# Kernel optimization log

Measured on AMD Instinct MI355X. Metric: run time of the kernel, lower is better.

Reference implementation:

```python
import jax, jax.numpy as jnp
import numpy as np

B, P, EPG = 1000, 100, 1200  # graphs, nodes/graph, edges/graph
IN, HID, OUT, K = 16, 64, 5, 3


def setup_inputs() -> dict:
    key = jax.random.key(0)
    ks = jax.random.split(key, 12)
    offs = jnp.repeat(jnp.arange(B, dtype=jnp.int32) * P, EPG)
    src = jax.random.randint(ks[0], (B * EPG,), 0, P, dtype=jnp.int32) + offs
    dst = jax.random.randint(ks[1], (B * EPG,), 0, P, dtype=jnp.int32) + offs
    graph_ids = jnp.repeat(jnp.arange(B, dtype=jnp.int32), P)
    feat = jax.random.normal(ks[2], (B * P, IN), dtype=jnp.float32)

    def lin(k1, fan_in, fan_out):
        s = 1.0 / np.sqrt(fan_in)
        return jax.random.uniform(k1, (fan_in, fan_out), jnp.float32, -s, s)

    return {
        'feat': feat, 'src': src, 'dst': dst, 'graph_ids': graph_ids,
        'n_graphs': B,
        'W1': lin(ks[3], K * IN, HID), 'b1': jnp.zeros((HID,), jnp.float32),
        'W2': lin(ks[4], K * HID, HID), 'b2': jnp.zeros((HID,), jnp.float32),
        'W3': lin(ks[5], K * HID, HID), 'b3': jnp.zeros((HID,), jnp.float32),
        'Wfc': lin(ks[6], HID, OUT), 'bfc': jnp.zeros((OUT,), jnp.float32),
    }


def _cheb_conv(x, src, dst, d_invsqrt, W, b, k):
    # DGL ChebConv with lambda_max=2 -> re_norm=1, scaled Laplacian = -D^-1/2 A D^-1/2
    n = x.shape[0]

    def Ax(h):
        msg = (h * d_invsqrt)[src]                      # gather from source nodes
        agg = jax.ops.segment_sum(msg, dst, num_segments=n)
        return agg * d_invsqrt

    Xs = [x]
    if k > 1:
        Xs.append(-Ax(Xs[0]))                           # X1 = L_hat X0
        for _ in range(2, k):
            Xs.append(-2.0 * Ax(Xs[-1]) - Xs[-2])       # X_i = 2 L_hat X_{i-1} - X_{i-2}
    Xt = jnp.concatenate(Xs, axis=1)                    # [n, k*f]
    return Xt @ W + b


def reference(feat, src, dst, graph_ids, n_graphs, W1, b1, W2, b2, W3, b3, Wfc, bfc):
    n = feat.shape[0]
    deg = jax.ops.segment_sum(jnp.ones((src.shape[0],), feat.dtype), dst, num_segments=n)
    d_invsqrt = jnp.where(deg < 1.0, 1.0, deg) ** -0.5
    d_invsqrt = d_invsqrt[:, None]

    h = jax.nn.relu(_cheb_conv(feat, src, dst, d_invsqrt, W1, b1, K))
    h = jax.nn.relu(_cheb_conv(h, src, dst, d_invsqrt, W2, b2, K))
    h = jax.nn.relu(_cheb_conv(h, src, dst, d_invsqrt, W3, b3, K))

    # dgl.mean_nodes: per-graph mean pooling
    counts = jax.ops.segment_sum(jnp.ones((n,), h.dtype), graph_ids, num_segments=n_graphs)
    hg = jax.ops.segment_sum(h, graph_ids, num_segments=n_graphs) / counts[:, None]
    return hg @ Wfc + bfc
```

## Files before the change

kernel.cpp:

```cpp
#include <hip/hip_runtime.h>

#define NGRAPH 1000
#define P      100
#define EPG    1200
#define INF    16
#define HID    64
#define NOUT   5

#define ASTR   88
#define T2OFF  72
#define SLOTA  64
#define SLOTB  80
#define NPAD   112


typedef short short8 __attribute__((ext_vector_type(8)));
typedef float f32x4  __attribute__((ext_vector_type(4)));

__device__ __forceinline__ void bsplit(float x, short& h, short& l) {
    unsigned u = __float_as_uint(x);
    h = (short)(u >> 16);
    float hf = __uint_as_float(u & 0xffff0000u);
    l = (short)(__float_as_uint(x - hf) >> 16);
}

__global__ __launch_bounds__(256) void wprep(
    const float* __restrict__ W1, const float* __restrict__ W2,
    const float* __restrict__ W3, short* __restrict__ wt)
{
    const int i0 = blockIdx.x * blockDim.x + threadIdx.x;
    const int stride = gridDim.x * blockDim.x;
    for (int e = i0; e < HID * 56; e += stride) {
        int c = e / 56, r = e % 56;
        float v = (r < 48) ? W1[r * HID + c] : 0.f;
        short h, l; bsplit(v, h, l);
        wt[e]        = h;
        wt[3584 + e] = l;
    }
    for (int e = i0; e < HID * 200; e += stride) {
        int c = e / 200, r = e % 200;
        float v2 = (r < 192) ? W2[r * HID + c] : 0.f;
        float v3 = (r < 192) ? W3[r * HID + c] : 0.f;
        short h, l;
        bsplit(v2, h, l); wt[7168 + e]  = h; wt[19968 + e] = l;
        bsplit(v3, h, l); wt[32768 + e] = h; wt[45568 + e] = l;
    }
}

__device__ __forceinline__ void prop_x1(
    float* __restrict__ A, int soff, int dslot,
    const unsigned char* __restrict__ csr_src,
    const int* __restrict__ csr_off,
    const float* __restrict__ dinv, int tid)
{
    const int q4 = (tid & 1) * 4;
    const int n  = tid >> 1;
    if (n < P) {
        const int kb = csr_off[n], ke = csr_off[n + 1];
        float ax = 0.f, ay = 0.f, az = 0.f, aw = 0.f;
        for (int k = kb; k < ke; k++) {
            int s = csr_src[k];
            const float4 x = *(const float4*)&A[s * ASTR + soff + q4];
            ax += x.x; ay += x.y; az += x.z; aw += x.w;
        }
        float dn = dinv[n];
        float m = -dn * dn;
        float4 o; o.x = m * ax; o.y = m * ay; o.z = m * az; o.w = m * aw;
        *(float4*)&A[n * ASTR + dslot + q4] = o;
    }
}

__device__ __forceinline__ void prop_dual(
    float* __restrict__ A, int t1c, int t1n, int ycur, int ynext, bool pre,
    const unsigned char* __restrict__ csr_src,
    const int* __restrict__ csr_off,
    const float* __restrict__ dinv, int tid)
{
    const int q4 = (tid & 1) * 4;
    const int n  = tid >> 1;
    if (n < P) {
        const int kb = csr_off[n], ke = csr_off[n + 1];
        float4 a2 = make_float4(0.f, 0.f, 0.f, 0.f);
        float4 a1 = make_float4(0.f, 0.f, 0.f, 0.f);
        if (pre) {
            for (int k = kb; k < ke; k++) {
                int s = csr_src[k];
                const float* rp = &A[s * ASTR + q4];
                const float4 x2 = *(const float4*)&rp[t1c];
                const float4 x1 = *(const float4*)&rp[ynext];
                a2.x += x2.x; a2.y += x2.y; a2.z += x2.z; a2.w += x2.w;
                a1.x += x1.x; a1.y += x1.y; a1.z += x1.z; a1.w += x1.w;
            }
        } else {
            for (int k = kb; k < ke; k++) {
                int s = csr_src[k];
                const float4 x2 = *(const float4*)&A[s * ASTR + t1c + q4];
                a2.x += x2.x; a2.y += x2.y; a2.z += x2.z; a2.w += x2.w;
            }
        }
        float dn = dinv[n];
        float d2 = dn * dn;
        const float4 y0 = *(const float4*)&A[n * ASTR + ycur + q4];
        float4 o2;
        float m2 = -2.f * d2;
        o2.x = m2 * a2.x - y0.x; o2.y = m2 * a2.y - y0.y;
        o2.z = m2 * a2.z - y0.z; o2.w = m2 * a2.w - y0.w;
        *(float4*)&A[n * ASTR + T2OFF + q4] = o2;
        if (pre) {
            float m1 = -d2;
            float4 o1;
            o1.x = m1 * a1.x; o1.y = m1 * a1.y;
            o1.z = m1 * a1.z; o1.w = m1 * a1.w;
            *(float4*)&A[n * ASTR + t1n + q4] = o1;
        }
    }
}

template <int F, int FINAL>
__device__ __forceinline__ void cheb_layer(
    float* __restrict__ A,
    const unsigned char* __restrict__ csr_src,
    const int* __restrict__ csr_off,
    const float* __restrict__ dinv,
    const short* __restrict__ whi, const short* __restrict__ wlo,
    const float* __restrict__ bias, int tid)
{
    const int RK   = 3 * F + 8;
    const int lane = tid & 63;
    const int wv   = tid >> 6;
    const int n16  = lane & 15;
    const int q    = lane >> 4;
    const int ncol = (wv << 4) + n16;

    f32x4 acc[7];
#pragma unroll
    for (int t = 0; t < 7; t++) { acc[t][0]=0.f; acc[t][1]=0.f; acc[t][2]=0.f; acc[t][3]=0.f; }

    prop_x1(A, 0, SLOTA, csr_src, csr_off, dinv, tid);
    __syncthreads();

    int t1c = SLOTA, t1n = SLOTB;
    for (int cb = 0; cb < F; cb += 8) {
        const bool pre = (cb + 8 < F);
        prop_dual(A, t1c, t1n, cb, cb + 8, pre, csr_src, csr_off, dinv, tid);
        __syncthreads();

        const int wr = (q == 0) ? cb : (q == 1) ? (F + cb)
                     : (q == 2) ? (2 * F + cb) : (3 * F);
        const short8 bhi = *(const short8*)&whi[ncol * RK + wr];
        const short8 blo = *(const short8*)&wlo[ncol * RK + wr];

        const int aoff = (q == 0) ? cb : (q == 1) ? t1c
                       : (q == 2) ? T2OFF : cb;
#pragma unroll
        for (int t = 0; t < 7; t++) {
            const float* xp = &A[(t * 16 + n16) * ASTR + aoff];
            const float4 v0 = *(const float4*)xp;
            const float4 v1 = *(const float4*)(xp + 4);
            short8 ahi, alo; short h, l;
            bsplit(v0.x, h, l); ahi[0] = h; alo[0] = l;
            bsplit(v0.y, h, l); ahi[1] = h; alo[1] = l;
            bsplit(v0.z, h, l); ahi[2] = h; alo[2] = l;
            bsplit(v0.w, h, l); ahi[3] = h; alo[3] = l;
            bsplit(v1.x, h, l); ahi[4] = h; alo[4] = l;
            bsplit(v1.y, h, l); ahi[5] = h; alo[5] = l;
            bsplit(v1.z, h, l); ahi[6] = h; alo[6] = l;
            bsplit(v1.w, h, l); ahi[7] = h; alo[7] = l;
            acc[t] = __builtin_amdgcn_mfma_f32_16x16x32_bf16(ahi, bhi, acc[t], 0, 0, 0);
            acc[t] = __builtin_amdgcn_mfma_f32_16x16x32_bf16(ahi, blo, acc[t], 0, 0, 0);
            acc[t] = __builtin_amdgcn_mfma_f32_16x16x32_bf16(alo, bhi, acc[t], 0, 0, 0);
        }
        __syncthreads();
        int tt = t1c; t1c = t1n; t1n = tt;
    }

    const float bcol = bias[ncol];
    const int rbase = q * 4;
#pragma unroll
    for (int t = 0; t < 7; t++) {
#pragma unroll
        for (int r = 0; r < 4; r++) {
            int row = t * 16 + rbase + r;
            if (row < P) {
                float dn = dinv[row];
                float v = acc[t][r];
                float o;
                if (FINAL) o = fmaxf(v * (1.0f / dn) + bcol, 0.f);
                else       o = fmaxf(v + bcol * dn, 0.f);
                A[row * ASTR + ncol] = o;
            }
        }
    }
    __syncthreads();
}

__global__ __launch_bounds__(256, 4) void gnn_kernel(
    const float* __restrict__ feat,
    const int* __restrict__ src, const int* __restrict__ dst,
    const float* __restrict__ b1, const float* __restrict__ b2,
    const float* __restrict__ b3,
    const float* __restrict__ Wfc, const float* __restrict__ bfc,
    const short* __restrict__ wt,
    float* __restrict__ out)
{
    __shared__ __align__(16) float A[NPAD * ASTR];
    __shared__ unsigned char csr_src[EPG];

    const int g = blockIdx.x;
    const int tid = threadIdx.x;
    const int base = g * P;
    const int* srcg = src + g * EPG;
    const int* dstg = dst + g * EPG;

    int*   deg     = (int*)&A[P * ASTR];
    int*   cur     = (int*)&A[P * ASTR + 100];
    int*   csr_off = (int*)&A[P * ASTR + 200];
    float* dinv    = &A[P * ASTR + 304];
    float* psum    = &A[P * ASTR + 404];

    for (int i = tid; i < P; i += 256) deg[i] = 0;
    __syncthreads();
    for (int e = tid; e < EPG; e += 256) {
        int d = dstg[e] - base;
        atomicAdd(&deg[d], 1);
    }
    __syncthreads();

    for (int i = tid; i < P; i += 256) {
        int dg = deg[i] > 1 ? deg[i] : 1;
        dinv[i] = rsqrtf((float)dg);
    }
    if (tid == 0) {
        int run = 0;
        csr_off[0] = 0;
        for (int i = 0; i < P; i++) { run += deg[i]; csr_off[i + 1] = run; }
    }
    __syncthreads();

    for (int i = tid; i < P * INF / 4; i += 256) {
        int n = i >> 2, fq = (i & 3) * 4;
        float4 v = *(const float4*)&feat[(size_t)base * INF + i * 4];
        float dn = dinv[n];
        v.x *= dn; v.y *= dn; v.z *= dn; v.w *= dn;
        *(float4*)&A[n * ASTR + fq] = v;
    }
    for (int i = tid; i < P; i += 256) cur[i] = csr_off[i];
    __syncthreads();
    for (int e = tid; e < EPG; e += 256) {
        int s = srcg[e] - base;
        int d = dstg[e] - base;
        int pos = atomicAdd(&cur[d], 1);
        csr_src[pos] = (unsigned char)s;
    }
    __syncthreads();

    cheb_layer<INF, 0>(A, csr_src, csr_off, dinv, wt,         wt + 3584,  b1, tid);
    cheb_layer<HID, 0>(A, csr_src, csr_off, dinv, wt + 7168,  wt + 19968, b2, tid);
    cheb_layer<HID, 1>(A, csr_src, csr_off, dinv, wt + 32768, wt + 45568, b3, tid);

    {
        const int lane = tid & 63, w = tid >> 6;
        float s = 0.f;
        for (int n = w; n < P; n += 4) s += A[n * ASTR + lane];
        psum[w * 64 + lane] = s;
    }
    __syncthreads();
    if (tid < HID) {
        float hg = (psum[tid] + psum[64 + tid] + psum[128 + tid] + psum[192 + tid]) * (1.0f / P);
        psum[256 + tid] = hg;
    }
    __syncthreads();
    if (tid < NOUT) {
        float o = bfc[tid];
        for (int c = 0; c < HID; c++) o += psum[256 + c] * Wfc[c * NOUT + tid];
        out[g * NOUT + tid] = o;
    }
}

extern "C" void kernel_launch(void* const* d_in, const int* in_sizes, int n_in,
                              void* d_out, int out_size, void* d_ws, size_t ws_size,
                              hipStream_t stream)
{
    const float* feat = (const float*)d_in[0];
    const int*   src  = (const int*)d_in[1];
    const int*   dst  = (const int*)d_in[2];
    const float* W1  = (const float*)d_in[5];
    const float* b1  = (const float*)d_in[6];
    const float* W2  = (const float*)d_in[7];
    const float* b2  = (const float*)d_in[8];
    const float* W3  = (const float*)d_in[9];
    const float* b3  = (const float*)d_in[10];
    const float* Wfc = (const float*)d_in[11];
    const float* bfc = (const float*)d_in[12];
    float* out = (float*)d_out;
    short* wt = (short*)d_ws;

    wprep<<<64, 256, 0, stream>>>(W1, W2, W3, wt);
    gnn_kernel<<<NGRAPH, 256, 0, stream>>>(feat, src, dst,
                                           b1, b2, b3, Wfc, bfc, wt, out);
}
```

Baseline: 186.8 us.

## Replace CSR sparse propagation with dense per-graph adjacency MFMA products

A new kernel builds each graph's dense 100x128 adjacency count matrix as bf16 in global workspace. The main kernel then computes the Laplacian propagation as MFMA matrix products against split-bf16 features instead of per-node CSR gather loops. Propagation now runs in 16-column chunks with an enlarged shared row stride that also holds degree and dinv, dropping the CSR build and the serial prefix scan. The cost is about 25 MB of extra adjacency traffic through global memory, an extra launch, and more MFMA work on a mostly zero matrix.

```diff
diff --git a/kernel.cpp b/kernel.cpp
--- a/kernel.cpp
+++ b/kernel.cpp
@@ -7,12 +7,25 @@
 #define HID    64
 #define NOUT   5
 
-#define ASTR   88
-#define T2OFF  72
-#define SLOTA  64
-#define SLOTB  80
-#define NPAD   112
-
+
+#define ASTR   100
+#define DINVC  64
+#define DEGC   65
+#define T1OFF  68
+#define T2OFF  84
+
+#define AINT_K   128
+#define AINT_SZ  (P * AINT_K)
+
+#define RK1    64
+#define RK2    208
+#define L1HI   0
+#define L1LO   4096
+#define L2HI   8192
+#define L2LO   21504
+#define L3HI   34816
+#define L3LO   48128
+#define WT_SHORTS 61440
 
 typedef short short8 __attribute__((ext_vector_type(8)));
 typedef float f32x4  __attribute__((ext_vector_type(4)));
@@ -30,160 +43,179 @@
 {
     const int i0 = blockIdx.x * blockDim.x + threadIdx.x;
     const int stride = gridDim.x * blockDim.x;
-    for (int e = i0; e < HID * 56; e += stride) {
-        int c = e / 56, r = e % 56;
-        float v = (r < 48) ? W1[r * HID + c] : 0.f;
+    for (int e = i0; e < HID * RK1; e += stride) {
+        int c = e / RK1, r = e % RK1;
+        float v = (r < 3 * INF) ? W1[r * HID + c] : 0.f;
         short h, l; bsplit(v, h, l);
-        wt[e]        = h;
-        wt[3584 + e] = l;
-    }
-    for (int e = i0; e < HID * 200; e += stride) {
-        int c = e / 200, r = e % 200;
-        float v2 = (r < 192) ? W2[r * HID + c] : 0.f;
-        float v3 = (r < 192) ? W3[r * HID + c] : 0.f;
+        wt[L1HI + e] = h;
+        wt[L1LO + e] = l;
+    }
+    for (int e = i0; e < HID * RK2; e += stride) {
+        int c = e / RK2, r = e % RK2;
+        float v2 = (r < 3 * HID) ? W2[r * HID + c] : 0.f;
+        float v3 = (r < 3 * HID) ? W3[r * HID + c] : 0.f;
         short h, l;
-        bsplit(v2, h, l); wt[7168 + e]  = h; wt[19968 + e] = l;
-        bsplit(v3, h, l); wt[32768 + e] = h; wt[45568 + e] = l;
-    }
-}
-
-__device__ __forceinline__ void prop_x1(
-    float* __restrict__ A, int soff, int dslot,
-    const unsigned char* __restrict__ csr_src,
-    const int* __restrict__ csr_off,
-    const float* __restrict__ dinv, int tid)
-{
-    const int q4 = (tid & 1) * 4;
-    const int n  = tid >> 1;
-    if (n < P) {
-        const int kb = csr_off[n], ke = csr_off[n + 1];
-        float ax = 0.f, ay = 0.f, az = 0.f, aw = 0.f;
-        for (int k = kb; k < ke; k++) {
-            int s = csr_src[k];
-            const float4 x = *(const float4*)&A[s * ASTR + soff + q4];
-            ax += x.x; ay += x.y; az += x.z; aw += x.w;
-        }
-        float dn = dinv[n];
-        float m = -dn * dn;
-        float4 o; o.x = m * ax; o.y = m * ay; o.z = m * az; o.w = m * aw;
-        *(float4*)&A[n * ASTR + dslot + q4] = o;
-    }
-}
-
-__device__ __forceinline__ void prop_dual(
-    float* __restrict__ A, int t1c, int t1n, int ycur, int ynext, bool pre,
-    const unsigned char* __restrict__ csr_src,
-    const int* __restrict__ csr_off,
-    const float* __restrict__ dinv, int tid)
-{
-    const int q4 = (tid & 1) * 4;
-    const int n  = tid >> 1;
-    if (n < P) {
-        const int kb = csr_off[n], ke = csr_off[n + 1];
-        float4 a2 = make_float4(0.f, 0.f, 0.f, 0.f);
-        float4 a1 = make_float4(0.f, 0.f, 0.f, 0.f);
-        if (pre) {
-            for (int k = kb; k < ke; k++) {
-                int s = csr_src[k];
-                const float* rp = &A[s * ASTR + q4];
-                const float4 x2 = *(const float4*)&rp[t1c];
-                const float4 x1 = *(const float4*)&rp[ynext];
-                a2.x += x2.x; a2.y += x2.y; a2.z += x2.z; a2.w += x2.w;
-                a1.x += x1.x; a1.y += x1.y; a1.z += x1.z; a1.w += x1.w;
+        bsplit(v2, h, l); wt[L2HI + e] = h; wt[L2LO + e] = l;
+        bsplit(v3, h, l); wt[L3HI + e] = h; wt[L3LO + e] = l;
+    }
+}
+
+__global__ __launch_bounds__(256) void abuild(
+    const int* __restrict__ src, const int* __restrict__ dst,
+    short* __restrict__ aint)
+{
+    __shared__ unsigned int cnt[AINT_SZ / 2];
+    const int g = blockIdx.x, tid = threadIdx.x, base = g * P;
+    for (int i = tid; i < AINT_SZ / 2; i += 256) cnt[i] = 0u;
+    __syncthreads();
+    const int* srcg = src + g * EPG;
+    const int* dstg = dst + g * EPG;
+    for (int e = tid; e < EPG; e += 256) {
+        int s = srcg[e] - base;
+        int d = dstg[e] - base;
+        int idx = d * AINT_K + s;
+        atomicAdd(&cnt[idx >> 1], 1u << ((idx & 1) * 16));
+    }
+    __syncthreads();
+    unsigned int* outw = (unsigned int*)(aint + (size_t)g * AINT_SZ);
+    for (int i = tid; i < AINT_SZ / 2; i += 256) {
+        unsigned int u = cnt[i];
+        unsigned int b0 = __float_as_uint((float)(u & 0xffffu)) >> 16;
+        unsigned int b1 = __float_as_uint((float)(u >> 16)) >> 16;
+        outw[i] = b0 | (b1 << 16);
+    }
+}
+
+template <int SECOND>
+__device__ __forceinline__ void dense_prop(
+    float* __restrict__ A, const short* __restrict__ aintg,
+    int arow0, int arow1, bool has2,
+    int srcoff, int dstoff, int ycol,
+    int rb0, int rb1, f32x4 dv0, f32x4 dv1, int lane)
+{
+    const int n16 = lane & 15;
+    const int q   = lane >> 4;
+    const int kq  = q * 8;
+    f32x4 p0, p1;
+    p0[0]=0.f; p0[1]=0.f; p0[2]=0.f; p0[3]=0.f;
+    p1[0]=0.f; p1[1]=0.f; p1[2]=0.f; p1[3]=0.f;
+#pragma unroll
+    for (int k = 0; k < 4; k++) {
+        const short8 a0 = *(const short8*)&aintg[arow0 * AINT_K + k * 32 + kq];
+        const short8 a1 = *(const short8*)&aintg[arow1 * AINT_K + k * 32 + kq];
+        short8 bhi, blo; short h, l;
+#pragma unroll
+        for (int j = 0; j < 8; j++) {
+            int row = k * 32 + kq + j;
+            if (k == 3) row = (row < P) ? row : 0;
+            float x = A[row * ASTR + srcoff + n16];
+            bsplit(x, h, l); bhi[j] = h; blo[j] = l;
+        }
+        p0 = __builtin_amdgcn_mfma_f32_16x16x32_bf16(a0, bhi, p0, 0, 0, 0);
+        p0 = __builtin_amdgcn_mfma_f32_16x16x32_bf16(a0, blo, p0, 0, 0, 0);
+        if (has2) {
+            p1 = __builtin_amdgcn_mfma_f32_16x16x32_bf16(a1, bhi, p1, 0, 0, 0);
+            p1 = __builtin_amdgcn_mfma_f32_16x16x32_bf16(a1, blo, p1, 0, 0, 0);
+        }
+    }
+#pragma unroll
+    for (int r = 0; r < 4; r++) {
+        const int row = rb0 + q * 4 + r;
+        const float d2 = dv0[r] * dv0[r];
+        float o;
+        if (SECOND) o = -2.f * d2 * p0[r] - A[row * ASTR + ycol];
+        else        o = -d2 * p0[r];
+        A[row * ASTR + dstoff + n16] = o;
+    }
+    if (has2) {
+#pragma unroll
+        for (int r = 0; r < 4; r++) {
+            const int row = rb1 + q * 4 + r;
+            if (rb1 != 84 || row >= 96) {
+                const float d2 = dv1[r] * dv1[r];
+                float o;
+                if (SECOND) o = -2.f * d2 * p1[r] - A[row * ASTR + ycol];
+                else        o = -d2 * p1[r];
+                A[row * ASTR + dstoff + n16] = o;
             }
-        } else {
-            for (int k = kb; k < ke; k++) {
-                int s = csr_src[k];
-                const float4 x2 = *(const float4*)&A[s * ASTR + t1c + q4];
-                a2.x += x2.x; a2.y += x2.y; a2.z += x2.z; a2.w += x2.w;
-            }
-        }
-        float dn = dinv[n];
-        float d2 = dn * dn;
-        const float4 y0 = *(const float4*)&A[n * ASTR + ycur + q4];
-        float4 o2;
-        float m2 = -2.f * d2;
-        o2.x = m2 * a2.x - y0.x; o2.y = m2 * a2.y - y0.y;
-        o2.z = m2 * a2.z - y0.z; o2.w = m2 * a2.w - y0.w;
-        *(float4*)&A[n * ASTR + T2OFF + q4] = o2;
-        if (pre) {
-            float m1 = -d2;
-            float4 o1;
-            o1.x = m1 * a1.x; o1.y = m1 * a1.y;
-            o1.z = m1 * a1.z; o1.w = m1 * a1.w;
-            *(float4*)&A[n * ASTR + t1n + q4] = o1;
         }
     }
 }
 
 template <int F, int FINAL>
 __device__ __forceinline__ void cheb_layer(
-    float* __restrict__ A,
-    const unsigned char* __restrict__ csr_src,
-    const int* __restrict__ csr_off,
-    const float* __restrict__ dinv,
+    float* __restrict__ A, const short* __restrict__ aintg,
     const short* __restrict__ whi, const short* __restrict__ wlo,
-    const float* __restrict__ bias, int tid)
-{
-    const int RK   = 3 * F + 8;
+    const float* __restrict__ bias,
+    int tid, int rb0, int rb1, bool has2, f32x4 dv0, f32x4 dv1)
+{
+    const int RK   = 3 * F + 16;
     const int lane = tid & 63;
     const int wv   = tid >> 6;
     const int n16  = lane & 15;
     const int q    = lane >> 4;
     const int ncol = (wv << 4) + n16;
 
+    const int arow0 = rb0 + n16;
+    const int arow1 = (has2 ? rb1 : rb0) + n16;
+
     f32x4 acc[7];
 #pragma unroll
     for (int t = 0; t < 7; t++) { acc[t][0]=0.f; acc[t][1]=0.f; acc[t][2]=0.f; acc[t][3]=0.f; }
 
-    prop_x1(A, 0, SLOTA, csr_src, csr_off, dinv, tid);
-    __syncthreads();
-
-    int t1c = SLOTA, t1n = SLOTB;
-    for (int cb = 0; cb < F; cb += 8) {
-        const bool pre = (cb + 8 < F);
-        prop_dual(A, t1c, t1n, cb, cb + 8, pre, csr_src, csr_off, dinv, tid);
+    for (int cb = 0; cb < F; cb += 16) {
+        dense_prop<0>(A, aintg, arow0, arow1, has2, cb, T1OFF, cb + n16,
+                      rb0, rb1, dv0, dv1, lane);
         __syncthreads();
-
-        const int wr = (q == 0) ? cb : (q == 1) ? (F + cb)
-                     : (q == 2) ? (2 * F + cb) : (3 * F);
-        const short8 bhi = *(const short8*)&whi[ncol * RK + wr];
-        const short8 blo = *(const short8*)&wlo[ncol * RK + wr];
-
-        const int aoff = (q == 0) ? cb : (q == 1) ? t1c
-                       : (q == 2) ? T2OFF : cb;
-#pragma unroll
-        for (int t = 0; t < 7; t++) {
-            const float* xp = &A[(t * 16 + n16) * ASTR + aoff];
-            const float4 v0 = *(const float4*)xp;
-            const float4 v1 = *(const float4*)(xp + 4);
-            short8 ahi, alo; short h, l;
-            bsplit(v0.x, h, l); ahi[0] = h; alo[0] = l;
-            bsplit(v0.y, h, l); ahi[1] = h; alo[1] = l;
-            bsplit(v0.z, h, l); ahi[2] = h; alo[2] = l;
-            bsplit(v0.w, h, l); ahi[3] = h; alo[3] = l;
-            bsplit(v1.x, h, l); ahi[4] = h; alo[4] = l;
-            bsplit(v1.y, h, l); ahi[5] = h; alo[5] = l;
-            bsplit(v1.z, h, l); ahi[6] = h; alo[6] = l;
-            bsplit(v1.w, h, l); ahi[7] = h; alo[7] = l;
-            acc[t] = __builtin_amdgcn_mfma_f32_16x16x32_bf16(ahi, bhi, acc[t], 0, 0, 0);
-            acc[t] = __builtin_amdgcn_mfma_f32_16x16x32_bf16(ahi, blo, acc[t], 0, 0, 0);
-            acc[t] = __builtin_amdgcn_mfma_f32_16x16x32_bf16(alo, bhi, acc[t], 0, 0, 0);
-        }
+        dense_prop<1>(A, aintg, arow0, arow1, has2, T1OFF, T2OFF, cb + n16,
+                      rb0, rb1, dv0, dv1, lane);
         __syncthreads();
-        int tt = t1c; t1c = t1n; t1n = tt;
+
+#pragma unroll
+        for (int ks = 0; ks < 2; ks++) {
+            int wr, aoff;
+            if (ks == 0) {
+                wr   = (q == 0) ? cb : (q == 1) ? cb + 8 : (q == 2) ? F + cb : F + cb + 8;
+                aoff = (q == 0) ? cb : (q == 1) ? cb + 8 : (q == 2) ? T1OFF  : T1OFF + 8;
+            } else {
+                wr   = (q == 0) ? 2*F + cb : (q == 1) ? 2*F + cb + 8 : (q == 2) ? 3*F : 3*F + 8;
+                aoff = (q == 0) ? T2OFF    : (q == 1) ? T2OFF + 8    : (q == 2) ? T1OFF : T1OFF + 8;
+            }
+            const short8 bhi = *(const short8*)&whi[ncol * RK + wr];
+            const short8 blo = *(const short8*)&wlo[ncol * RK + wr];
+#pragma unroll
+            for (int t = 0; t < 7; t++) {
+                const int row = ((t < 6) ? t * 16 : 84) + n16;
+                const float* xp = &A[row * ASTR + aoff];
+                const float4 v0 = *(const float4*)xp;
+                const float4 v1 = *(const float4*)(xp + 4);
+                short8 ahi, alo; short h, l;
+                bsplit(v0.x, h, l); ahi[0] = h; alo[0] = l;
+                bsplit(v0.y, h, l); ahi[1] = h; alo[1] = l;
+                bsplit(v0.z, h, l); ahi[2] = h; alo[2] = l;
+                bsplit(v0.w, h, l); ahi[3] = h; alo[3] = l;
+                bsplit(v1.x, h, l); ahi[4] = h; alo[4] = l;
+                bsplit(v1.y, h, l); ahi[5] = h; alo[5] = l;
+                bsplit(v1.z, h, l); ahi[6] = h; alo[6] = l;
+                bsplit(v1.w, h, l); ahi[7] = h; alo[7] = l;
+                acc[t] = __builtin_amdgcn_mfma_f32_16x16x32_bf16(ahi, bhi, acc[t], 0, 0, 0);
+                acc[t] = __builtin_amdgcn_mfma_f32_16x16x32_bf16(ahi, blo, acc[t], 0, 0, 0);
+                acc[t] = __builtin_amdgcn_mfma_f32_16x16x32_bf16(alo, bhi, acc[t], 0, 0, 0);
+            }
+        }
+        __syncthreads();
     }
 
     const float bcol = bias[ncol];
-    const int rbase = q * 4;
 #pragma unroll
     for (int t = 0; t < 7; t++) {
+        const int rbase = ((t < 6) ? t * 16 : 84) + q * 4;
 #pragma unroll
         for (int r = 0; r < 4; r++) {
-            int row = t * 16 + rbase + r;
-            if (row < P) {
-                float dn = dinv[row];
-                float v = acc[t][r];
+            const int row = rbase + r;
+            if (t < 6 || row >= 96) {
+                const float dn = A[row * ASTR + DINVC];
+                const float v = acc[t][r];
                 float o;
                 if (FINAL) o = fmaxf(v * (1.0f / dn) + bcol, 0.f);
                 else       o = fmaxf(v + bcol * dn, 0.f);
@@ -200,79 +232,70 @@
     const float* __restrict__ b1, const float* __restrict__ b2,
     const float* __restrict__ b3,
     const float* __restrict__ Wfc, const float* __restrict__ bfc,
-    const short* __restrict__ wt,
+    const short* __restrict__ wt, const short* __restrict__ aint,
     float* __restrict__ out)
 {
-    __shared__ __align__(16) float A[NPAD * ASTR];
-    __shared__ unsigned char csr_src[EPG];
-
+    __shared__ __align__(16) float A[P * ASTR];
     const int g = blockIdx.x;
     const int tid = threadIdx.x;
     const int base = g * P;
-    const int* srcg = src + g * EPG;
     const int* dstg = dst + g * EPG;
 
-    int*   deg     = (int*)&A[P * ASTR];
-    int*   cur     = (int*)&A[P * ASTR + 100];
-    int*   csr_off = (int*)&A[P * ASTR + 200];
-    float* dinv    = &A[P * ASTR + 304];
-    float* psum    = &A[P * ASTR + 404];
-
-    for (int i = tid; i < P; i += 256) deg[i] = 0;
+    for (int i = tid; i < P; i += 256) *(int*)&A[i * ASTR + DEGC] = 0;
     __syncthreads();
     for (int e = tid; e < EPG; e += 256) {
         int d = dstg[e] - base;
-        atomicAdd(&deg[d], 1);
-    }
-    __syncthreads();
-
+        atomicAdd((int*)&A[d * ASTR + DEGC], 1);
+    }
+    __syncthreads();
     for (int i = tid; i < P; i += 256) {
-        int dg = deg[i] > 1 ? deg[i] : 1;
-        dinv[i] = rsqrtf((float)dg);
-    }
-    if (tid == 0) {
-        int run = 0;
-        csr_off[0] = 0;
-        for (int i = 0; i < P; i++) { run += deg[i]; csr_off[i + 1] = run; }
+        int dg = *(int*)&A[i * ASTR + DEGC];
+        A[i * ASTR + DINVC] = rsqrtf((float)(dg > 1 ? dg : 1));
     }
     __syncthreads();
 
     for (int i = tid; i < P * INF / 4; i += 256) {
         int n = i >> 2, fq = (i & 3) * 4;
         float4 v = *(const float4*)&feat[(size_t)base * INF + i * 4];
-        float dn = dinv[n];
+        float dn = A[n * ASTR + DINVC];
         v.x *= dn; v.y *= dn; v.z *= dn; v.w *= dn;
         *(float4*)&A[n * ASTR + fq] = v;
     }
-    for (int i = tid; i < P; i += 256) cur[i] = csr_off[i];
-    __syncthreads();
-    for (int e = tid; e < EPG; e += 256) {
-        int s = srcg[e] - base;
-        int d = dstg[e] - base;
-        int pos = atomicAdd(&cur[d], 1);
-        csr_src[pos] = (unsigned char)s;
-    }
-    __syncthreads();
-
-    cheb_layer<INF, 0>(A, csr_src, csr_off, dinv, wt,         wt + 3584,  b1, tid);
-    cheb_layer<HID, 0>(A, csr_src, csr_off, dinv, wt + 7168,  wt + 19968, b2, tid);
-    cheb_layer<HID, 1>(A, csr_src, csr_off, dinv, wt + 32768, wt + 45568, b3, tid);
+    __syncthreads();
+
+    const int lane = tid & 63, wv = tid >> 6, q = lane >> 4;
+    const int rb0 = wv * 16;
+    const int t2i = wv + 4;
+    const int rb1 = (t2i >= 6) ? 84 : t2i * 16;
+    const bool has2 = (wv < 3);
+    f32x4 dv0, dv1;
+#pragma unroll
+    for (int r = 0; r < 4; r++) {
+        dv0[r] = A[(rb0 + q * 4 + r) * ASTR + DINVC];
+        dv1[r] = A[((has2 ? rb1 : rb0) + q * 4 + r) * ASTR + DINVC];
+    }
+
+    const short* aintg = aint + (size_t)g * AINT_SZ;
+    cheb_layer<INF, 0>(A, aintg, wt + L1HI, wt + L1LO, b1, tid, rb0, rb1, has2, dv0, dv1);
+    cheb_layer<HID, 0>(A, aintg, wt + L2HI, wt + L2LO, b2, tid, rb0, rb1, has2, dv0, dv1);
+    cheb_layer<HID, 1>(A, aintg, wt + L3HI, wt + L3LO, b3, tid, rb0, rb1, has2, dv0, dv1);
 
     {
-        const int lane = tid & 63, w = tid >> 6;
+        const int l2 = tid & 63, w = tid >> 6;
         float s = 0.f;
-        for (int n = w; n < P; n += 4) s += A[n * ASTR + lane];
-        psum[w * 64 + lane] = s;
+        for (int n = w; n < P; n += 4) s += A[n * ASTR + l2];
+        A[l2 * ASTR + T1OFF + w] = s;
     }
     __syncthreads();
     if (tid < HID) {
-        float hg = (psum[tid] + psum[64 + tid] + psum[128 + tid] + psum[192 + tid]) * (1.0f / P);
-        psum[256 + tid] = hg;
+        float hg = (A[tid * ASTR + T1OFF] + A[tid * ASTR + T1OFF + 1] +
+                    A[tid * ASTR + T1OFF + 2] + A[tid * ASTR + T1OFF + 3]) * (1.0f / P);
+        A[tid * ASTR + T1OFF + 4] = hg;
     }
     __syncthreads();
     if (tid < NOUT) {
         float o = bfc[tid];
-        for (int c = 0; c < HID; c++) o += psum[256 + c] * Wfc[c * NOUT + tid];
+        for (int c = 0; c < HID; c++) o += A[c * ASTR + T1OFF + 4] * Wfc[c * NOUT + tid];
         out[g * NOUT + tid] = o;
     }
 }
@@ -293,9 +316,12 @@
     const float* Wfc = (const float*)d_in[11];
     const float* bfc = (const float*)d_in[12];
     float* out = (float*)d_out;
-    short* wt = (short*)d_ws;
+
+    short* wt   = (short*)d_ws;
+    short* aint = wt + WT_SHORTS;
 
     wprep<<<64, 256, 0, stream>>>(W1, W2, W3, wt);
+    abuild<<<NGRAPH, 256, 0, stream>>>(src, dst, aint);
     gnn_kernel<<<NGRAPH, 256, 0, stream>>>(feat, src, dst,
-                                           b1, b2, b3, Wfc, bfc, wt, out);
-}
+                                           b1, b2, b3, Wfc, bfc, wt, aint, out);
+}
```

New measurement: 161.7 us. -13.4%, faster.
